# Kernel tuning notes

Measured on AMD Instinct MI355X. Metric: run time of the kernel, lower is better.

Reference implementation:

```python
import jax, jax.numpy as jnp
import numpy as np

SPLINE_ORDER = 3
GRID_SIZE = 1
# efficient-kan style grid over [-1,1], extended by spline_order on each side; h = 2/grid_size = 2
GRID = jnp.arange(-SPLINE_ORDER, GRID_SIZE + SPLINE_ORDER + 1, dtype=jnp.float32) * 2.0 - 1.0
NB = GRID_SIZE + SPLINE_ORDER  # 4 basis functions per input feature
EPS = 1e-5


def b_splines(x, grid):
    # x: [..., in] -> [..., in, NB] via Cox-de Boor recursion
    xe = x[..., None]
    b = ((xe >= grid[:-1]) & (xe < grid[1:])).astype(x.dtype)
    for p in range(1, SPLINE_ORDER + 1):
        b = ((xe - grid[:-(p + 1)]) / (grid[p:-1] - grid[:-(p + 1)]) * b[..., :-1]
             + (grid[p + 1:] - xe) / (grid[p + 1:] - grid[1:-p]) * b[..., 1:])
    return b


def kan_linear(x, base_w, spline_w):
    # base branch: silu(x) @ W_base^T ; spline branch: B(x) contracted with W_spline [out,in,NB]
    base = jnp.einsum('...i,oi->...o', jax.nn.silu(x), base_w)
    sp = jnp.einsum('...ik,oik->...o', b_splines(x, GRID), spline_w)
    return base + sp


def kan_conv2x2(x, base_w, spline_w):
    # x: [B,C,H,W] -> [B,C_out,H-1,W-1]
    p = jax.lax.conv_general_dilated_patches(x, (2, 2), (1, 1), 'VALID')  # [B, C*4, H', W']
    p = jnp.moveaxis(p, 1, -1)  # [B,H',W',C*4]
    y = kan_linear(p, base_w, spline_w)  # [B,H',W',C_out]
    return jnp.moveaxis(y, -1, 1)


def bn2d(x, g, b):
    m = x.mean((0, 2, 3), keepdims=True)
    v = x.var((0, 2, 3), keepdims=True)
    return (x - m) * jax.lax.rsqrt(v + EPS) * g[None, :, None, None] + b[None, :, None, None]


def bn1d(x, g, b):
    m = x.mean(0, keepdims=True)
    v = x.var(0, keepdims=True)
    return (x - m) * jax.lax.rsqrt(v + EPS) * g[None, :] + b[None, :]


def maxpool2(x):
    B, C, H, W = x.shape
    Hc, Wc = (H // 2) * 2, (W // 2) * 2
    return x[:, :, :Hc, :Wc].reshape(B, C, H // 2, 2, W // 2, 2).max((3, 5))


def setup_inputs() -> dict:
    key = jax.random.key(0)
    ks = jax.random.split(key, 16)
    f32 = jnp.float32
    d = {
        'x': jax.random.normal(ks[0], (1024, 3, 32, 32), f32),
        'base_w1': jax.random.normal(ks[1], (32, 12), f32) * 0.2,
        'spline_w1': jax.random.normal(ks[2], (32, 12, NB), f32) * 0.1,
        'bn1_g': jnp.ones((32,), f32), 'bn1_b': jnp.zeros((32,), f32),
        'base_w2': jax.random.normal(ks[3], (64, 128), f32) * 0.08,
        'spline_w2': jax.random.normal(ks[4], (64, 128, NB), f32) * 0.04,
        'bn2_g': jnp.ones((64,), f32), 'bn2_b': jnp.zeros((64,), f32),
        'fc1_w': jax.random.normal(ks[5], (64, 3136), f32) * 0.02,
        'fc1_b': jnp.zeros((64,), f32),
        'bn3_g': jnp.ones((64,), f32), 'bn3_b': jnp.zeros((64,), f32),
        'fc2_w': jax.random.normal(ks[6], (10, 64), f32) * 0.1,
        'fc2_b': jnp.zeros((10,), f32),
    }
    return d


def reference(x, base_w1, spline_w1, bn1_g, bn1_b, base_w2, spline_w2, bn2_g, bn2_b,
              fc1_w, fc1_b, bn3_g, bn3_b, fc2_w, fc2_b):
    h = kan_conv2x2(x, base_w1, spline_w1)            # [B,32,31,31]
    h = jax.nn.relu(bn2d(h, bn1_g, bn1_b))
    h = maxpool2(h)                                   # [B,32,15,15]
    h = kan_conv2x2(h, base_w2, spline_w2)            # [B,64,14,14]
    h = jax.nn.relu(bn2d(h, bn2_g, bn2_b))
    h = maxpool2(h)                                   # [B,64,7,7]
    h = h.reshape(h.shape[0], -1)                     # [B,3136]
    h = h @ fc1_w.T + fc1_b
    h = jax.nn.relu(bn1d(h, bn3_g, bn3_b))
    # Dropout is identity at inference
    return h @ fc2_w.T + fc2_b                        # [B,10]
```

## Files before the change

### kernel.cpp

```cpp
#include <hip/hip_runtime.h>
#include <math.h>

#define BN_EPS 1e-5f

typedef __attribute__((ext_vector_type(8))) _Float16 f16x8;
typedef __attribute__((ext_vector_type(4))) _Float16 f16x4;
typedef __attribute__((ext_vector_type(2))) __fp16 fp16v2;
typedef __attribute__((ext_vector_type(4))) float f32x4;


__device__ __forceinline__ float siluf(float v) {
    return v * __builtin_amdgcn_rcpf(1.0f + __expf(-v));
}

__device__ __forceinline__ void expand5(float v, float f[5]) {
    f[0] = siluf(v);
    float u = (v + 7.0f) * 0.5f;
#pragma unroll
    for (int i = 0; i < 4; ++i) {
        float a = fabsf(u - (float)(i + 2));
        float p = fmaxf(2.0f - a, 0.0f);
        float q = fmaxf(1.0f - a, 0.0f);
        f[i + 1] = p * p * p - 4.0f * (q * q * q);
    }
}

__device__ __forceinline__ int pkh(float a, float b) {
    union { fp16v2 h2; int i; } u;
    u.h2 = __builtin_amdgcn_cvt_pkrtz(a, b);
    return u.i;
}


__global__ __launch_bounds__(256) void wconv1h_kernel(
        const float* __restrict__ bw, const float* __restrict__ sw,
        _Float16* __restrict__ Wf1) {
    int t = blockIdx.x * 256 + threadIdx.x;
    if (t >= 32 * 64) return;
    int n = t >> 6;
    int k = t & 63;
    int s = k >> 4, j = k & 15;
    float val = 0.f;
    if (j < 15) {
        int f = j / 3, c = j - f * 3;
        int i = c * 4 + s;
        val = (f == 0) ? bw[n * 12 + i]
                       : sw[(n * 12 + i) * 4 + f - 1] * (1.0f / 6.0f);
    }
    Wf1[t] = (_Float16)val;
}


#define C1_LDW 24

__global__ __launch_bounds__(256, 8) void conv1_kernel(
        const float* __restrict__ x, const _Float16* __restrict__ Wf1,
        _Float16* __restrict__ pooled, float* __restrict__ part) {
    __shared__ _Float16 Eu[82 * C1_LDW];
    __shared__ float Rs[4][64];

    int t = threadIdx.x;
    int lane = t & 63, wv = t >> 6;
    int quad = lane >> 4, l15 = lane & 15;

    int blk = blockIdx.x;
    int b = blk >> 4;
    int ty = (blk >> 2) & 3, tx = blk & 3;

    const _Float16* wb0 = Wf1 + (size_t)l15 * 64 + quad * 8;
    f16x8 bf00 = *(const f16x8*)(wb0);
    f16x8 bf01 = *(const f16x8*)(wb0 + 32);
    f16x8 bf10 = *(const f16x8*)(wb0 + 16 * 64);
    f16x8 bf11 = *(const f16x8*)(wb0 + 16 * 64 + 32);

    if (t < 243) {
        int c = t / 81;
        int pos = t - c * 81;
        int yy = pos / 9, xx = pos - yy * 9;
        int Y = ty * 8 + yy, X = tx * 8 + xx;
        float v = 0.f;
        if (Y < 32 && X < 32)
            v = x[((size_t)(b * 3 + c)) * 1024 + Y * 32 + X];
        float f[5];
        expand5(v, f);
        _Float16* eb = &Eu[pos * C1_LDW + c];
        eb[0]  = (_Float16)f[0];
        eb[3]  = (_Float16)f[1];
        eb[6]  = (_Float16)f[2];
        eb[9]  = (_Float16)f[3];
        eb[12] = (_Float16)f[4];
    }
    if (t < 24) Eu[81 * C1_LDW + t] = (_Float16)0.f;

    int wy = 2 * wv + (l15 >> 3), wx = l15 & 7;
    bool valid = (ty * 8 + wy < 31) && (tx * 8 + wx < 31);
    int dxq = quad >> 1, hq = (quad & 1) * 8;
    int p0 = valid ? (wy * 9 + wx + dxq) * C1_LDW + hq : 81 * C1_LDW + hq;
    int p1 = valid ? ((wy + 1) * 9 + wx + dxq) * C1_LDW + hq : 81 * C1_LDW + hq;
    __syncthreads();

    f32x4 acc0 = (f32x4){0.f, 0.f, 0.f, 0.f};
    f32x4 acc1 = (f32x4){0.f, 0.f, 0.f, 0.f};
    f16x8 a0 = *(const f16x8*)&Eu[p0];
    acc0 = __builtin_amdgcn_mfma_f32_16x16x32_f16(a0, bf00, acc0, 0, 0, 0);
    acc1 = __builtin_amdgcn_mfma_f32_16x16x32_f16(a0, bf10, acc1, 0, 0, 0);
    f16x8 a1 = *(const f16x8*)&Eu[p1];
    acc0 = __builtin_amdgcn_mfma_f32_16x16x32_f16(a1, bf01, acc0, 0, 0, 0);
    acc1 = __builtin_amdgcn_mfma_f32_16x16x32_f16(a1, bf11, acc1, 0, 0, 0);

    float h00 = fmaxf(acc0[0], acc0[1]);
    float h01 = fmaxf(acc0[2], acc0[3]);
    float h10 = fmaxf(acc1[0], acc1[1]);
    float h11 = fmaxf(acc1[2], acc1[3]);
    float g00 = fmaxf(h00, __shfl_down(h00, 32, 64));
    float g01 = fmaxf(h01, __shfl_down(h01, 32, 64));
    float g10 = fmaxf(h10, __shfl_down(h10, 32, 64));
    float g11 = fmaxf(h11, __shfl_down(h11, 32, 64));
    if (lane < 32) {
        int pm = 4 * ty + wv;
        int pn0 = 4 * tx + (quad & 1) * 2;
        if (pm < 15) {
            size_t base = ((size_t)b * 225 + pm * 15) * 32;
            if (pn0 < 15) {
                pooled[base + pn0 * 32 + l15]      = (_Float16)g00;
                pooled[base + pn0 * 32 + 16 + l15] = (_Float16)g10;
            }
            if (pn0 + 1 < 15) {
                pooled[base + (pn0 + 1) * 32 + l15]      = (_Float16)g01;
                pooled[base + (pn0 + 1) * 32 + 16 + l15] = (_Float16)g11;
            }
        }
    }

    float s0 = acc0[0] + acc0[1] + acc0[2] + acc0[3];
    float q0 = acc0[0] * acc0[0] + acc0[1] * acc0[1]
             + acc0[2] * acc0[2] + acc0[3] * acc0[3];
    float s1 = acc1[0] + acc1[1] + acc1[2] + acc1[3];
    float q1 = acc1[0] * acc1[0] + acc1[1] * acc1[1]
             + acc1[2] * acc1[2] + acc1[3] * acc1[3];
    s0 += __shfl_down(s0, 32, 64); s0 += __shfl_down(s0, 16, 64);
    q0 += __shfl_down(q0, 32, 64); q0 += __shfl_down(q0, 16, 64);
    s1 += __shfl_down(s1, 32, 64); s1 += __shfl_down(s1, 16, 64);
    q1 += __shfl_down(q1, 32, 64); q1 += __shfl_down(q1, 16, 64);
    if (lane < 16) {
        Rs[wv][2 * l15]          = s0;
        Rs[wv][2 * l15 + 1]      = q0;
        Rs[wv][32 + 2 * l15]     = s1;
        Rs[wv][32 + 2 * l15 + 1] = q1;
    }
    __syncthreads();
    if (t < 64)
        part[(size_t)blk * 64 + t] = Rs[0][t] + Rs[1][t] + Rs[2][t] + Rs[3][t];
}


__global__ __launch_bounds__(256) void wconv16_kernel(
        const float* __restrict__ bw, const float* __restrict__ sw,
        _Float16* __restrict__ Wf) {
    int t = blockIdx.x * 256 + threadIdx.x;
    if (t >= 64 * 640) return;
    int n = t / 640;
    int k = t - n * 640;
    int s = k / 160;
    int r = k - s * 160;
    int f = r >> 5;
    int c = r & 31;
    float val = (f == 0) ? bw[n * 128 + c * 4 + s]
                         : sw[n * 512 + c * 16 + s * 4 + (f - 1)] * (1.0f / 6.0f);
    Wf[t] = (_Float16)val;
}


#define EU_LDW 168

__device__ __forceinline__ void c2_loadb(const _Float16* __restrict__ Wb,
                                         int g, f16x8 bf[5]) {
#pragma unroll
    for (int ks = 0; ks < 5; ++ks)
        bf[ks] = *(const f16x8*)(Wb + g * 160 + ks * 32);
}

__device__ __forceinline__ void c2_mfma(const _Float16* Eu,
                                        const int abase[4][4], int g,
                                        int quad, const f16x8 bf[5],
                                        f32x4 acc[4]) {
#pragma unroll
    for (int ks = 0; ks < 5; ++ks) {
        int jo = ks * 32 + quad * 8;
#pragma unroll
        for (int mt = 0; mt < 4; ++mt) {
            f16x8 a = *(const f16x8*)&Eu[abase[mt][g] + jo];
            acc[mt] = __builtin_amdgcn_mfma_f32_16x16x32_f16(a, bf[ks], acc[mt], 0, 0, 0);
        }
    }
}

__global__ __launch_bounds__(256, 6) void conv2_kernel(
        const _Float16* __restrict__ pooled, const float* __restrict__ stats1,
        const float* __restrict__ g1v, const float* __restrict__ b1v,
        const _Float16* __restrict__ Wf, _Float16* __restrict__ Pt,
        float* __restrict__ part) {
    __shared__ _Float16 Eu[65 * EU_LDW];

    int t = threadIdx.x;
    int lane = t & 63, wv = t >> 6;
    int quad = lane >> 4, l15 = lane & 15;

    int blk = blockIdx.x;
    int b = blk >> 2;
    int py0 = ((blk >> 1) & 1) * 7;
    int px0 = (blk & 1) * 7;

    const _Float16* Wb = Wf + (size_t)(wv * 16 + l15) * 640 + quad * 8;
    f16x8 bfA[5], bfB[5];
    c2_loadb(Wb, 0, bfA);

    {
        int c2 = t & 15, c0 = c2 * 2;
        int yr = (t >> 4) & 7;
        int xh = t >> 7;
        const float invN1 = 1.0f / (1024.0f * 961.0f);
        float m0 = stats1[2 * c0] * invN1;
        float v0 = stats1[2 * c0 + 1] * invN1 - m0 * m0;
        float sc0 = rsqrtf(v0 + BN_EPS) * g1v[c0];
        float sh0 = b1v[c0] - m0 * sc0;
        float m1 = stats1[2 * c0 + 2] * invN1;
        float v1 = stats1[2 * c0 + 3] * invN1 - m1 * m1;
        float sc1 = rsqrtf(v1 + BN_EPS) * g1v[c0 + 1];
        float sh1 = b1v[c0 + 1] - m1 * sc1;
        const _Float16* prow =
            pooled + ((size_t)b * 225 + (py0 + yr) * 15 + px0) * 32 + c0;
#pragma unroll
        for (int xi = 0; xi < 4; ++xi) {
            int xx = xh * 4 + xi;
            fp16v2 v2 = *(const fp16v2*)(prow + xx * 32);
            float va = fmaxf((float)v2.x * sc0 + sh0, 0.f);
            float vb = fmaxf((float)v2.y * sc1 + sh1, 0.f);
            float fa[5], fb5[5];
            expand5(va, fa);
            expand5(vb, fb5);
            int* eb = (int*)&Eu[(yr * 8 + xx) * EU_LDW + c0];
            eb[0]  = pkh(fa[0], fb5[0]);
            eb[16] = pkh(fa[1], fb5[1]);
            eb[32] = pkh(fa[2], fb5[2]);
            eb[48] = pkh(fa[3], fb5[3]);
            eb[64] = pkh(fa[4], fb5[4]);
        }
    }
    if (t < 84) *(int*)((char*)&Eu[64 * EU_LDW] + t * 4) = 0;

    int abase[4][4];
#pragma unroll
    for (int mt = 0; mt < 4; ++mt) {
        int m = mt * 16 + l15;
        if (m < 49) {
            int pr = m / 7, pc = m - pr * 7;
#pragma unroll
            for (int s = 0; s < 4; ++s)
                abase[mt][s] = ((pr + (s >> 1)) * 8 + pc + (s & 1)) * EU_LDW;
        } else {
#pragma unroll
            for (int s = 0; s < 4; ++s) abase[mt][s] = 64 * EU_LDW;
        }
    }
    __syncthreads();

    f32x4 acc[4];
#pragma unroll
    for (int mt = 0; mt < 4; ++mt) acc[mt] = (f32x4){0.f, 0.f, 0.f, 0.f};

    c2_loadb(Wb, 1, bfB);
    c2_mfma(Eu, abase, 0, quad, bfA, acc);
    c2_loadb(Wb, 2, bfA);
    c2_mfma(Eu, abase, 1, quad, bfB, acc);
    c2_loadb(Wb, 3, bfB);
    c2_mfma(Eu, abase, 2, quad, bfA, acc);
    c2_mfma(Eu, abase, 3, quad, bfB, acc);

    int o = wv * 16 + l15;
#pragma unroll
    for (int mt = 0; mt < 4; ++mt) {
#pragma unroll
        for (int reg = 0; reg < 4; ++reg) {
            int m = mt * 16 + quad * 4 + reg;
            if (m < 49) {
                int pr = m / 7, pc = m - pr * 7;
                int patch = (b * 14 + py0 + pr) * 14 + px0 + pc;
                Pt[(size_t)patch * 64 + o] = (_Float16)acc[mt][reg];
            }
        }
    }
    float s = 0.f, s2 = 0.f;
#pragma unroll
    for (int mt = 0; mt < 4; ++mt)
#pragma unroll
        for (int reg = 0; reg < 4; ++reg) {
            float a = acc[mt][reg];
            s += a;
            s2 += a * a;
        }
    s  += __shfl_down(s, 16, 64);  s  += __shfl_down(s, 32, 64);
    s2 += __shfl_down(s2, 16, 64); s2 += __shfl_down(s2, 32, 64);
    if (lane < 16) {
        part[(size_t)blk * 128 + 2 * o]     = s;
        part[(size_t)blk * 128 + 2 * o + 1] = s2;
    }
}


__global__ __launch_bounds__(256) void redstats_kernel(
        const float* __restrict__ part, float* __restrict__ stats,
        int nblk, int stride) {
    int p = blockIdx.x;
    float s = 0.f;
    for (int j = threadIdx.x; j < nblk; j += 256)
        s += part[(size_t)j * stride + p];
#pragma unroll
    for (int off = 32; off > 0; off >>= 1) s += __shfl_down(s, off, 64);
    __shared__ float ls[4];
    if ((threadIdx.x & 63) == 0) ls[threadIdx.x >> 6] = s;
    __syncthreads();
    if (threadIdx.x == 0) stats[p] = ls[0] + ls[1] + ls[2] + ls[3];
}


__global__ __launch_bounds__(256) void bnpool2_kernel(
        const _Float16* __restrict__ Pt, const float* __restrict__ stats,
        const float* __restrict__ g, const float* __restrict__ bb,
        _Float16* __restrict__ out) {
    int t = blockIdx.x * 256 + threadIdx.x;
    if (t >= 1024 * 49 * 16) return;
    int c4 = (t & 15) * 4;
    int q2 = (t >> 4) % 49;
    int b  = t / (49 * 16);
    float sc[4], sh[4];
#pragma unroll
    for (int j = 0; j < 4; ++j) {
        int c = c4 + j;
        float mean = stats[2 * c] * (1.0f / 200704.0f);
        float var  = stats[2 * c + 1] * (1.0f / 200704.0f) - mean * mean;
        sc[j] = rsqrtf(var + BN_EPS) * g[c];
        sh[j] = bb[c] - mean * sc[j];
    }
    int py2 = q2 / 7, px2 = q2 - py2 * 7;
    int q = (py2 * 2) * 14 + px2 * 2;
    const _Float16* p = Pt + ((size_t)b * 196 + q) * 64 + c4;
    f16x4 r0 = *(const f16x4*)(p);
    f16x4 r1 = *(const f16x4*)(p + 64);
    f16x4 r2 = *(const f16x4*)(p + 14 * 64);
    f16x4 r3 = *(const f16x4*)(p + 15 * 64);
    f16x4 res;
#pragma unroll
    for (int j = 0; j < 4; ++j) {
        float v0 = fmaxf((float)r0[j] * sc[j] + sh[j], 0.f);
        float v1 = fmaxf((float)r1[j] * sc[j] + sh[j], 0.f);
        float v2 = fmaxf((float)r2[j] * sc[j] + sh[j], 0.f);
        float v3 = fmaxf((float)r3[j] * sc[j] + sh[j], 0.f);
        res[j] = (_Float16)fmaxf(fmaxf(v0, v1), fmaxf(v2, v3));
    }
    *(f16x4*)(out + (size_t)b * 3136 + q2 * 64 + c4) = res;
}


__global__ __launch_bounds__(256) void transpose_kernel(
        const float* __restrict__ w, unsigned int* __restrict__ wTh2) {
    int t = blockIdx.x * 256 + threadIdx.x;
    if (t >= 64 * 1568) return;
    int o = t & 63;
    int j2 = t >> 6;
    int jc = (j2 * 2) & 63;
    int q2 = (j2 * 2) >> 6;
    wTh2[t] = (unsigned int)pkh(w[(size_t)o * 3136 + jc * 49 + q2],
                                w[(size_t)o * 3136 + (jc + 1) * 49 + q2]);
}


__global__ __launch_bounds__(256) void fc1_kernel(
        const _Float16* __restrict__ xin, const unsigned int* __restrict__ wTh2,
        const float* __restrict__ bias, float* __restrict__ z) {
    __shared__ unsigned int xsu[4 * 1568];
    __shared__ float red[4][4][64];
    int b0 = blockIdx.x * 4;
    const unsigned int* xg = (const unsigned int*)xin + (size_t)b0 * 1568;
    for (int j = threadIdx.x; j < 4 * 1568; j += 256) xsu[j] = xg[j];
    __syncthreads();
    int o = threadIdx.x & 63, q = threadIdx.x >> 6;
    float s0 = 0.f, s1 = 0.f, s2 = 0.f, s3 = 0.f;
    const unsigned int* wp = wTh2 + (size_t)q * 392 * 64 + o;
    int jb = q * 392;
    for (int i = 0; i < 392; ++i) {
        union { unsigned int u; fp16v2 h; } uw, u0, u1, u2, u3;
        uw.u = wp[i * 64];
        u0.u = xsu[jb + i];
        u1.u = xsu[1568 + jb + i];
        u2.u = xsu[2 * 1568 + jb + i];
        u3.u = xsu[3 * 1568 + jb + i];
        s0 = __builtin_amdgcn_fdot2(u0.h, uw.h, s0, false);
        s1 = __builtin_amdgcn_fdot2(u1.h, uw.h, s1, false);
        s2 = __builtin_amdgcn_fdot2(u2.h, uw.h, s2, false);
        s3 = __builtin_amdgcn_fdot2(u3.h, uw.h, s3, false);
    }
    red[0][q][o] = s0; red[1][q][o] = s1; red[2][q][o] = s2; red[3][q][o] = s3;
    __syncthreads();
    int bb = threadIdx.x >> 6;
    float tot = red[bb][0][o] + red[bb][1][o] + red[bb][2][o] + red[bb][3][o] + bias[o];
    z[((size_t)(b0 + bb)) * 64 + o] = tot;
}


__global__ __launch_bounds__(256) void colstats_kernel(
        const float* __restrict__ z, float* __restrict__ stats) {
    int c = blockIdx.x;
    float s = 0.f, s2 = 0.f;
    for (int b = threadIdx.x; b < 1024; b += 256) {
        float v = z[(size_t)b * 64 + c];
        s += v; s2 += v * v;
    }
#pragma unroll
    for (int off = 32; off > 0; off >>= 1) {
        s  += __shfl_down(s, off, 64);
        s2 += __shfl_down(s2, off, 64);
    }
    __shared__ float ls[8];
    int w = threadIdx.x >> 6;
    if ((threadIdx.x & 63) == 0) { ls[w * 2] = s; ls[w * 2 + 1] = s2; }
    __syncthreads();
    if (threadIdx.x == 0) {
        stats[2 * c]     = ls[0] + ls[2] + ls[4] + ls[6];
        stats[2 * c + 1] = ls[1] + ls[3] + ls[5] + ls[7];
    }
}


__global__ __launch_bounds__(256) void final_kernel(
        const float* __restrict__ z, const float* __restrict__ stats,
        const float* __restrict__ g, const float* __restrict__ bb,
        const float* __restrict__ w2, const float* __restrict__ b2,
        float* __restrict__ out) {
    int t = blockIdx.x * 256 + threadIdx.x;
    if (t >= 10240) return;
    int o = t % 10, b = t / 10;
    float acc = b2[o];
#pragma unroll 8
    for (int c = 0; c < 64; ++c) {
        float mean = stats[2 * c] * (1.0f / 1024.0f);
        float var  = stats[2 * c + 1] * (1.0f / 1024.0f) - mean * mean;
        float sc = rsqrtf(var + BN_EPS) * g[c];
        float a = fmaxf(z[(size_t)b * 64 + c] * sc + (bb[c] - mean * sc), 0.f);
        acc += a * w2[o * 64 + c];
    }
    out[t] = acc;
}


extern "C" void kernel_launch(void* const* d_in, const int* in_sizes, int n_in,
                              void* d_out, int out_size, void* d_ws, size_t ws_size,
                              hipStream_t stream) {
    const float* x   = (const float*)d_in[0];
    const float* bw1 = (const float*)d_in[1];
    const float* sw1 = (const float*)d_in[2];
    const float* g1  = (const float*)d_in[3];
    const float* b1  = (const float*)d_in[4];
    const float* bw2 = (const float*)d_in[5];
    const float* sw2 = (const float*)d_in[6];
    const float* g2  = (const float*)d_in[7];
    const float* b2v = (const float*)d_in[8];
    const float* fw1 = (const float*)d_in[9];
    const float* fb1 = (const float*)d_in[10];
    const float* g3  = (const float*)d_in[11];
    const float* b3  = (const float*)d_in[12];
    const float* fw2 = (const float*)d_in[13];
    const float* fb2 = (const float*)d_in[14];
    float* out = (float*)d_out;

    char* ws = (char*)d_ws;
    float* part1     = (float*)(ws);
    _Float16* Pt     = (_Float16*)(ws);
    float* part2     = (float*)(ws + 51380224);
    _Float16* Wf     = (_Float16*)(ws + 100000000);
    _Float16* Wf1    = (_Float16*)(ws + 100131072);
    _Float16* pooled = (_Float16*)(ws + 125960192);
    float* z         = (float*)(ws + 155451392);
    unsigned int* wTh2 = (unsigned int*)(ws + 155713536);
    float* stats1    = (float*)(ws + 156516352);
    float* stats2    = (float*)(ws + 156516608);
    float* stats3    = (float*)(ws + 156517120);

    transpose_kernel<<<392, 256, 0, stream>>>(fw1, wTh2);
    wconv16_kernel<<<160, 256, 0, stream>>>(bw2, sw2, Wf);
    wconv1h_kernel<<<8, 256, 0, stream>>>(bw1, sw1, Wf1);

    conv1_kernel<<<16384, 256, 0, stream>>>(x, Wf1, pooled, part1);
    redstats_kernel<<<64, 256, 0, stream>>>(part1, stats1, 16384, 64);

    conv2_kernel<<<4096, 256, 0, stream>>>(pooled, stats1, g1, b1,
                                           Wf, Pt, part2);
    redstats_kernel<<<128, 256, 0, stream>>>(part2, stats2, 4096, 128);

    _Float16* pooled2 = pooled;
    bnpool2_kernel<<<(1024 * 49 * 16 + 255) / 256, 256, 0, stream>>>(
        Pt, stats2, g2, b2v, pooled2);

    fc1_kernel<<<256, 256, 0, stream>>>(pooled2, wTh2, fb1, z);
    colstats_kernel<<<64, 256, 0, stream>>>(z, stats3);
    final_kernel<<<(10240 + 255) / 256, 256, 0, stream>>>(z, stats3, g3, b3, fw2, fb2, out);
}
```

Measured before the change: 235.0 us.

## Process whole image per block in conv1 with swizzled LDS and row loop

conv1 now assigns one full 32x32 image per block instead of 16 tiles. Each block expands the whole image into an XOR-swizzled shared buffer, then loops over 16 row-pairs, issuing MFMAs and accumulating BN statistics in registers. This removes the halo recomputation, cuts the partial-stats buffer from 16384 rows to 1024, and lowers launch overhead. The cost is more LDS and fewer resident blocks (launch bounds drop to 4), a serial row loop, and only 1024 blocks to fill the GPU. Smaller changes: conv2 switches its load loop from x to y with occupancy hint 7, and BN3 scale and shift are precomputed once in colstats instead of in every final_kernel thread.

```diff
diff --git a/kernel.cpp b/kernel.cpp
--- a/kernel.cpp
+++ b/kernel.cpp
@@ -51,21 +51,17 @@
 }
 
 
-#define C1_LDW 24
-
-__global__ __launch_bounds__(256, 8) void conv1_kernel(
+__global__ __launch_bounds__(256, 4) void conv1_kernel(
         const float* __restrict__ x, const _Float16* __restrict__ Wf1,
         _Float16* __restrict__ pooled, float* __restrict__ part) {
-    __shared__ _Float16 Eu[82 * C1_LDW];
+    __shared__ _Float16 Eu[1025 * 16];
     __shared__ float Rs[4][64];
+    char* EuB = (char*)Eu;
 
     int t = threadIdx.x;
     int lane = t & 63, wv = t >> 6;
     int quad = lane >> 4, l15 = lane & 15;
-
-    int blk = blockIdx.x;
-    int b = blk >> 4;
-    int ty = (blk >> 2) & 3, tx = blk & 3;
+    int b = blockIdx.x;
 
     const _Float16* wb0 = Wf1 + (size_t)l15 * 64 + quad * 8;
     f16x8 bf00 = *(const f16x8*)(wb0);
@@ -73,84 +69,99 @@
     f16x8 bf10 = *(const f16x8*)(wb0 + 16 * 64);
     f16x8 bf11 = *(const f16x8*)(wb0 + 16 * 64 + 32);
 
-    if (t < 243) {
-        int c = t / 81;
-        int pos = t - c * 81;
-        int yy = pos / 9, xx = pos - yy * 9;
-        int Y = ty * 8 + yy, X = tx * 8 + xx;
-        float v = 0.f;
-        if (Y < 32 && X < 32)
-            v = x[((size_t)(b * 3 + c)) * 1024 + Y * 32 + X];
+    float xv[12];
+    const float* xb = x + (size_t)b * 3072;
+#pragma unroll
+    for (int k = 0; k < 12; ++k) xv[k] = xb[t + k * 256];
+#pragma unroll
+    for (int k = 0; k < 12; ++k) {
+        int idx = t + k * 256;
+        int c = idx >> 10;
+        int pos = idx & 1023;
         float f[5];
-        expand5(v, f);
-        _Float16* eb = &Eu[pos * C1_LDW + c];
-        eb[0]  = (_Float16)f[0];
-        eb[3]  = (_Float16)f[1];
-        eb[6]  = (_Float16)f[2];
-        eb[9]  = (_Float16)f[3];
-        eb[12] = (_Float16)f[4];
-    }
-    if (t < 24) Eu[81 * C1_LDW + t] = (_Float16)0.f;
-
-    int wy = 2 * wv + (l15 >> 3), wx = l15 & 7;
-    bool valid = (ty * 8 + wy < 31) && (tx * 8 + wx < 31);
-    int dxq = quad >> 1, hq = (quad & 1) * 8;
-    int p0 = valid ? (wy * 9 + wx + dxq) * C1_LDW + hq : 81 * C1_LDW + hq;
-    int p1 = valid ? ((wy + 1) * 9 + wx + dxq) * C1_LDW + hq : 81 * C1_LDW + hq;
-    __syncthreads();
-
-    f32x4 acc0 = (f32x4){0.f, 0.f, 0.f, 0.f};
-    f32x4 acc1 = (f32x4){0.f, 0.f, 0.f, 0.f};
-    f16x8 a0 = *(const f16x8*)&Eu[p0];
-    acc0 = __builtin_amdgcn_mfma_f32_16x16x32_f16(a0, bf00, acc0, 0, 0, 0);
-    acc1 = __builtin_amdgcn_mfma_f32_16x16x32_f16(a0, bf10, acc1, 0, 0, 0);
-    f16x8 a1 = *(const f16x8*)&Eu[p1];
-    acc0 = __builtin_amdgcn_mfma_f32_16x16x32_f16(a1, bf01, acc0, 0, 0, 0);
-    acc1 = __builtin_amdgcn_mfma_f32_16x16x32_f16(a1, bf11, acc1, 0, 0, 0);
-
-    float h00 = fmaxf(acc0[0], acc0[1]);
-    float h01 = fmaxf(acc0[2], acc0[3]);
-    float h10 = fmaxf(acc1[0], acc1[1]);
-    float h11 = fmaxf(acc1[2], acc1[3]);
-    float g00 = fmaxf(h00, __shfl_down(h00, 32, 64));
-    float g01 = fmaxf(h01, __shfl_down(h01, 32, 64));
-    float g10 = fmaxf(h10, __shfl_down(h10, 32, 64));
-    float g11 = fmaxf(h11, __shfl_down(h11, 32, 64));
-    if (lane < 32) {
-        int pm = 4 * ty + wv;
-        int pn0 = 4 * tx + (quad & 1) * 2;
-        if (pm < 15) {
-            size_t base = ((size_t)b * 225 + pm * 15) * 32;
+        expand5(xv[k], f);
+        int rb = pos * 32;
+        int key = (pos & 12) << 2;
+        *(_Float16*)(EuB + ((rb + c * 2) ^ key))        = (_Float16)f[0];
+        *(_Float16*)(EuB + ((rb + (3 + c) * 2) ^ key))  = (_Float16)f[1];
+        *(_Float16*)(EuB + ((rb + (6 + c) * 2) ^ key))  = (_Float16)f[2];
+        *(_Float16*)(EuB + ((rb + (9 + c) * 2) ^ key))  = (_Float16)f[3];
+        *(_Float16*)(EuB + ((rb + (12 + c) * 2) ^ key)) = (_Float16)f[4];
+    }
+    if (t < 8) *(int*)(EuB + 32768 + t * 4) = 0;
+    __syncthreads();
+
+    int dxq = quad >> 1, hb = (quad & 1) * 16;
+    int wxv = 8 * wv + (l15 & 7);
+    int colb = wxv + dxq;
+    int pbase = (colb * 32 + hb) ^ ((colb & 12) << 2);
+    bool vx = wxv < 31;
+    int pzero = 32768 + hb;
+    int wy0 = l15 >> 3;
+
+    float ss0 = 0.f, sq0 = 0.f, ss1 = 0.f, sq1 = 0.f;
+
+    int wy = wy0;
+    int p0 = vx ? wy * 1024 + pbase : pzero;
+    f16x8 a0 = *(const f16x8*)(EuB + p0);
+    f16x8 a1 = *(const f16x8*)(EuB + p0 + (vx ? 1024 : 0));
+
+#pragma unroll 1
+    for (int i = 0; i < 16; ++i) {
+        f32x4 acc0 = (f32x4){0.f, 0.f, 0.f, 0.f};
+        f32x4 acc1 = (f32x4){0.f, 0.f, 0.f, 0.f};
+        acc0 = __builtin_amdgcn_mfma_f32_16x16x32_f16(a0, bf00, acc0, 0, 0, 0);
+        acc1 = __builtin_amdgcn_mfma_f32_16x16x32_f16(a0, bf10, acc1, 0, 0, 0);
+        acc0 = __builtin_amdgcn_mfma_f32_16x16x32_f16(a1, bf01, acc0, 0, 0, 0);
+        acc1 = __builtin_amdgcn_mfma_f32_16x16x32_f16(a1, bf11, acc1, 0, 0, 0);
+        if (i < 15) {
+            int wyn = 2 * (i + 1) + wy0;
+            bool vn = vx && (wyn < 31);
+            int pn = vn ? wyn * 1024 + pbase : pzero;
+            a0 = *(const f16x8*)(EuB + pn);
+            a1 = *(const f16x8*)(EuB + pn + (vn ? 1024 : 0));
+        }
+        float h00 = fmaxf(acc0[0], acc0[1]);
+        float h01 = fmaxf(acc0[2], acc0[3]);
+        float h10 = fmaxf(acc1[0], acc1[1]);
+        float h11 = fmaxf(acc1[2], acc1[3]);
+        float g00 = fmaxf(h00, __shfl_down(h00, 32, 64));
+        float g01 = fmaxf(h01, __shfl_down(h01, 32, 64));
+        float g10 = fmaxf(h10, __shfl_down(h10, 32, 64));
+        float g11 = fmaxf(h11, __shfl_down(h11, 32, 64));
+        if (lane < 32 && i < 15) {
+            int pn0 = 4 * wv + (quad & 1) * 2;
+            size_t base = ((size_t)b * 225 + i * 15) * 32;
             if (pn0 < 15) {
                 pooled[base + pn0 * 32 + l15]      = (_Float16)g00;
                 pooled[base + pn0 * 32 + 16 + l15] = (_Float16)g10;
             }
-            if (pn0 + 1 < 15) {
+            if (pn0 < 14) {
                 pooled[base + (pn0 + 1) * 32 + l15]      = (_Float16)g01;
                 pooled[base + (pn0 + 1) * 32 + 16 + l15] = (_Float16)g11;
             }
         }
-    }
-
-    float s0 = acc0[0] + acc0[1] + acc0[2] + acc0[3];
-    float q0 = acc0[0] * acc0[0] + acc0[1] * acc0[1]
+        ss0 += acc0[0] + acc0[1] + acc0[2] + acc0[3];
+        sq0 += acc0[0] * acc0[0] + acc0[1] * acc0[1]
              + acc0[2] * acc0[2] + acc0[3] * acc0[3];
-    float s1 = acc1[0] + acc1[1] + acc1[2] + acc1[3];
-    float q1 = acc1[0] * acc1[0] + acc1[1] * acc1[1]
+        ss1 += acc1[0] + acc1[1] + acc1[2] + acc1[3];
+        sq1 += acc1[0] * acc1[0] + acc1[1] * acc1[1]
              + acc1[2] * acc1[2] + acc1[3] * acc1[3];
-    s0 += __shfl_down(s0, 32, 64); s0 += __shfl_down(s0, 16, 64);
-    q0 += __shfl_down(q0, 32, 64); q0 += __shfl_down(q0, 16, 64);
-    s1 += __shfl_down(s1, 32, 64); s1 += __shfl_down(s1, 16, 64);
-    q1 += __shfl_down(q1, 32, 64); q1 += __shfl_down(q1, 16, 64);
+    }
+
+    ss0 += __shfl_down(ss0, 32, 64); ss0 += __shfl_down(ss0, 16, 64);
+    sq0 += __shfl_down(sq0, 32, 64); sq0 += __shfl_down(sq0, 16, 64);
+    ss1 += __shfl_down(ss1, 32, 64); ss1 += __shfl_down(ss1, 16, 64);
+    sq1 += __shfl_down(sq1, 32, 64); sq1 += __shfl_down(sq1, 16, 64);
     if (lane < 16) {
-        Rs[wv][2 * l15]          = s0;
-        Rs[wv][2 * l15 + 1]      = q0;
-        Rs[wv][32 + 2 * l15]     = s1;
-        Rs[wv][32 + 2 * l15 + 1] = q1;
+        Rs[wv][2 * l15]          = ss0;
+        Rs[wv][2 * l15 + 1]      = sq0;
+        Rs[wv][32 + 2 * l15]     = ss1;
+        Rs[wv][32 + 2 * l15 + 1] = sq1;
     }
     __syncthreads();
     if (t < 64)
-        part[(size_t)blk * 64 + t] = Rs[0][t] + Rs[1][t] + Rs[2][t] + Rs[3][t];
+        part[(size_t)b * 64 + t] = Rs[0][t] + Rs[1][t] + Rs[2][t] + Rs[3][t];
 }
 
 
@@ -195,7 +206,7 @@
     }
 }
 
-__global__ __launch_bounds__(256, 6) void conv2_kernel(
+__global__ __launch_bounds__(256, 7) void conv2_kernel(
         const _Float16* __restrict__ pooled, const float* __restrict__ stats1,
         const float* __restrict__ g1v, const float* __restrict__ b1v,
         const _Float16* __restrict__ Wf, _Float16* __restrict__ Pt,
@@ -217,8 +228,8 @@
 
     {
         int c2 = t & 15, c0 = c2 * 2;
-        int yr = (t >> 4) & 7;
-        int xh = t >> 7;
+        int xx = (t >> 4) & 7;
+        int yh = t >> 7;
         const float invN1 = 1.0f / (1024.0f * 961.0f);
         float m0 = stats1[2 * c0] * invN1;
         float v0 = stats1[2 * c0 + 1] * invN1 - m0 * m0;
@@ -228,12 +239,12 @@
         float v1 = stats1[2 * c0 + 3] * invN1 - m1 * m1;
         float sc1 = rsqrtf(v1 + BN_EPS) * g1v[c0 + 1];
         float sh1 = b1v[c0 + 1] - m1 * sc1;
-        const _Float16* prow =
-            pooled + ((size_t)b * 225 + (py0 + yr) * 15 + px0) * 32 + c0;
-#pragma unroll
-        for (int xi = 0; xi < 4; ++xi) {
-            int xx = xh * 4 + xi;
-            fp16v2 v2 = *(const fp16v2*)(prow + xx * 32);
+        const _Float16* pbase0 =
+            pooled + ((size_t)b * 225 + py0 * 15 + px0) * 32 + c0;
+#pragma unroll
+        for (int yi = 0; yi < 4; ++yi) {
+            int yr = yh * 4 + yi;
+            fp16v2 v2 = *(const fp16v2*)(pbase0 + yr * 480 + xx * 32);
             float va = fmaxf((float)v2.x * sc0 + sh0, 0.f);
             float vb = fmaxf((float)v2.y * sc1 + sh1, 0.f);
             float fa[5], fb5[5];
@@ -409,7 +420,8 @@
 
 
 __global__ __launch_bounds__(256) void colstats_kernel(
-        const float* __restrict__ z, float* __restrict__ stats) {
+        const float* __restrict__ z, const float* __restrict__ g,
+        const float* __restrict__ bb, float* __restrict__ scsh) {
     int c = blockIdx.x;
     float s = 0.f, s2 = 0.f;
     for (int b = threadIdx.x; b < 1024; b += 256) {
@@ -426,15 +438,19 @@
     if ((threadIdx.x & 63) == 0) { ls[w * 2] = s; ls[w * 2 + 1] = s2; }
     __syncthreads();
     if (threadIdx.x == 0) {
-        stats[2 * c]     = ls[0] + ls[2] + ls[4] + ls[6];
-        stats[2 * c + 1] = ls[1] + ls[3] + ls[5] + ls[7];
+        float st = ls[0] + ls[2] + ls[4] + ls[6];
+        float st2 = ls[1] + ls[3] + ls[5] + ls[7];
+        float mean = st * (1.0f / 1024.0f);
+        float var  = st2 * (1.0f / 1024.0f) - mean * mean;
+        float sc = rsqrtf(var + BN_EPS) * g[c];
+        scsh[2 * c]     = sc;
+        scsh[2 * c + 1] = bb[c] - mean * sc;
     }
 }
 
 
 __global__ __launch_bounds__(256) void final_kernel(
-        const float* __restrict__ z, const float* __restrict__ stats,
-        const float* __restrict__ g, const float* __restrict__ bb,
+        const float* __restrict__ z, const float* __restrict__ scsh,
         const float* __restrict__ w2, const float* __restrict__ b2,
         float* __restrict__ out) {
     int t = blockIdx.x * 256 + threadIdx.x;
@@ -443,10 +459,7 @@
     float acc = b2[o];
 #pragma unroll 8
     for (int c = 0; c < 64; ++c) {
-        float mean = stats[2 * c] * (1.0f / 1024.0f);
-        float var  = stats[2 * c + 1] * (1.0f / 1024.0f) - mean * mean;
-        float sc = rsqrtf(var + BN_EPS) * g[c];
-        float a = fmaxf(z[(size_t)b * 64 + c] * sc + (bb[c] - mean * sc), 0.f);
+        float a = fmaxf(z[(size_t)b * 64 + c] * scsh[2 * c] + scsh[2 * c + 1], 0.f);
         acc += a * w2[o * 64 + c];
     }
     out[t] = acc;
@@ -490,8 +503,8 @@
     wconv16_kernel<<<160, 256, 0, stream>>>(bw2, sw2, Wf);
     wconv1h_kernel<<<8, 256, 0, stream>>>(bw1, sw1, Wf1);
 
-    conv1_kernel<<<16384, 256, 0, stream>>>(x, Wf1, pooled, part1);
-    redstats_kernel<<<64, 256, 0, stream>>>(part1, stats1, 16384, 64);
+    conv1_kernel<<<1024, 256, 0, stream>>>(x, Wf1, pooled, part1);
+    redstats_kernel<<<64, 256, 0, stream>>>(part1, stats1, 1024, 64);
 
     conv2_kernel<<<4096, 256, 0, stream>>>(pooled, stats1, g1, b1,
                                            Wf, Pt, part2);
@@ -502,6 +515,6 @@
         Pt, stats2, g2, b2v, pooled2);
 
     fc1_kernel<<<256, 256, 0, stream>>>(pooled2, wTh2, fb1, z);
-    colstats_kernel<<<64, 256, 0, stream>>>(z, stats3);
-    final_kernel<<<(10240 + 255) / 256, 256, 0, stream>>>(z, stats3, g3, b3, fw2, fb2, out);
-}
+    colstats_kernel<<<64, 256, 0, stream>>>(z, g3, b3, stats3);
+    final_kernel<<<(10240 + 255) / 256, 256, 0, stream>>>(z, stats3, fw2, fb2, out);
+}
```

New measurement: 196.8 us. -16.3%, faster.
